# Optimization experiments

Hardware: AMD Instinct MI355X
Metric: run time of the kernel (lower is better)

Reference implementation:

```python
import jax, jax.numpy as jnp
import numpy as np

E = 8           # ensemble size
D_IN = 512      # input_dim (state+action)
H = 1024        # hidden size, arch=[1024, 1024]
D_OUT = 1       # output_dim (Q value)
LN_EPS = 1e-5


def setup_inputs() -> dict:
    key = jax.random.key(0)
    ks = jax.random.split(key, 8)
    s1 = 1.0 / np.sqrt(D_IN)
    s2 = 1.0 / np.sqrt(H)
    return {
        "x": jax.random.normal(ks[0], (16384, D_IN), dtype=jnp.float32),
        # stacked per-ensemble parameters: leading axis E
        "W1": jax.random.uniform(ks[1], (E, D_IN, H), jnp.float32, -s1, s1),
        "b1": jax.random.uniform(ks[2], (E, H), jnp.float32, -s1, s1),
        "g1": jnp.ones((E, H), jnp.float32),
        "be1": jnp.zeros((E, H), jnp.float32),
        "W2": jax.random.uniform(ks[3], (E, H, H), jnp.float32, -s2, s2),
        "b2": jax.random.uniform(ks[4], (E, H), jnp.float32, -s2, s2),
        "g2": jnp.ones((E, H), jnp.float32),
        "be2": jnp.zeros((E, H), jnp.float32),
        "W3": jax.random.uniform(ks[5], (E, H, D_OUT), jnp.float32, -s2, s2),
        "b3": jax.random.uniform(ks[6], (E, D_OUT), jnp.float32, -s2, s2),
    }


def _layer_norm(h, g, b):
    # h: [E, B, H]; g, b: [E, H] -> broadcast over batch
    mu = jnp.mean(h, axis=-1, keepdims=True)
    var = jnp.mean(jnp.square(h - mu), axis=-1, keepdims=True)
    return (h - mu) * jax.lax.rsqrt(var + LN_EPS) * g[:, None, :] + b[:, None, :]


def reference(x, W1, b1, g1, be1, W2, b2, g2, be2, W3, b3):
    # Layer 1: all ensemble members as one batched GEMM on shared input
    h = jnp.einsum('bd,edh->ebh', x, W1) + b1[:, None, :]       # [E, B, H]
    h = jax.nn.relu(_layer_norm(h, g1, be1))
    # Layer 2
    h = jnp.einsum('ebd,edh->ebh', h, W2) + b2[:, None, :]      # [E, B, H]
    h = jax.nn.relu(_layer_norm(h, g2, be2))
    # Head (identity head activation)
    qs = jnp.einsum('ebd,edo->ebo', h, W3) + b3[:, None, :]      # [E, B, 1]
    q = jnp.min(qs, axis=0)                                      # [B, 1]
    return (q, qs)
```

## Files before the change

### kernel.cpp

```cpp
#include <hip/hip_runtime.h>
#include <hip/hip_bf16.h>
#include <stdint.h>

#define EN    8
#define DIN   512
#define HID   1024
#define BATCH 16384
#define LN_EPS 1e-5f

typedef __bf16   bf16x8 __attribute__((ext_vector_type(8)));
typedef float    f32x4  __attribute__((ext_vector_type(4)));
typedef uint16_t u16x8  __attribute__((ext_vector_type(8)));
typedef uint16_t u16x4  __attribute__((ext_vector_type(4)));
typedef float    fl4    __attribute__((ext_vector_type(4)));

__device__ __forceinline__ uint16_t f2bf(float f) {
  uint32_t x = __builtin_bit_cast(uint32_t, f);
  uint32_t r = (x + 0x7fffu + ((x >> 16) & 1u)) >> 16;
  return (uint16_t)r;
}
__device__ __forceinline__ float bf2f(uint16_t u) {
  return __builtin_bit_cast(float, (uint32_t)u << 16);
}

__device__ __forceinline__ void gload16(const uint16_t* g, char* lds_d) {
  __builtin_amdgcn_global_load_lds(
      (const __attribute__((address_space(1))) uint32_t*)g,
      (__attribute__((address_space(3))) uint32_t*)lds_d, 16, 0, 0);
}

__device__ __forceinline__ f32x4 MF(bf16x8 a, bf16x8 b, f32x4 c) {
  return __builtin_amdgcn_mfma_f32_16x16x32_bf16(a, b, c, 0, 0, 0);
}

__global__ __launch_bounds__(256) void cvt_bf16(const float* __restrict__ src,
                                                uint16_t* __restrict__ dst, long n) {
  long i = ((long)blockIdx.x * 256 + threadIdx.x) * 4;
  if (i >= n) return;
  fl4 v = *(const fl4*)(src + i);
  u16x4 o;
  #pragma unroll
  for (int j = 0; j < 4; ++j) o[j] = f2bf(v[j]);
  *(u16x4*)(dst + i) = o;
}

__global__ __launch_bounds__(256) void transpose_cvt(const float* __restrict__ src,
                                                     uint16_t* __restrict__ dst,
                                                     int R, int C) {
  __shared__ float tile[32][33];
  const int e = blockIdx.z;
  const int c0 = blockIdx.x * 32;
  const int r0 = blockIdx.y * 32;
  const int tx = threadIdx.x & 31, ty = threadIdx.x >> 5;
  const float* s = src + (size_t)e * R * C;
  uint16_t*    d = dst + (size_t)e * R * C;
  #pragma unroll
  for (int i = 0; i < 32; i += 8)
    tile[ty + i][tx] = s[(size_t)(r0 + ty + i) * C + (c0 + tx)];
  __syncthreads();
  #pragma unroll
  for (int i = 0; i < 32; i += 8)
    d[(size_t)(c0 + ty + i) * R + (r0 + tx)] = f2bf(tile[tx][ty + i]);
}

__global__ __launch_bounds__(512, 2) void gemm256(
    const uint16_t* __restrict__ A, size_t a_estride,
    const uint16_t* __restrict__ Bt,
    const float*    __restrict__ bias,
    uint16_t*       __restrict__ C,
    int M, int K) {
  __shared__ __attribute__((aligned(16))) char lds[131072];
  const int tid = threadIdx.x;
  const int bx  = blockIdx.x;
  const int e   = bx & 7;
  const int t   = bx >> 3;
  const int mt  = t >> 2;
  const int nt  = t & 3;
  const int NT  = K >> 6;
  const int HT  = NT * 4;

  const uint16_t* Ae = A + (size_t)e * a_estride + (size_t)(mt * 256) * K;
  const uint16_t* Be = Bt + ((size_t)e * HID + nt * 256) * K;

  const int l  = tid & 63, wid = tid >> 6;
  const int wr = wid >> 2, wc = wid & 3;
  const int fr = l & 15, kq = l >> 4, f7 = fr & 7;

  const int srow = tid >> 3;
  const int su   = (tid & 7) ^ (srow & 7);
  const uint16_t* sA0 = Ae + (size_t)srow * K + su * 8;
  const uint16_t* sB0 = Be + (size_t)srow * K + su * 8;
  char* const dst0 = lds + tid * 16;

  const int rdA = wr * 8192 + fr * 128 + ((kq ^ f7) << 4);
  const int rdB = ((wc < 2) ? 16384 : 32768) + (wc & 1) * 8192 + fr * 128 + ((kq ^ f7) << 4);

  f32x4 acc[8][4];
  #pragma unroll
  for (int i = 0; i < 8; ++i)
    #pragma unroll
    for (int j = 0; j < 4; ++j) acc[i][j] = (f32x4)0.0f;

  auto STAGE = [&](int H) {
    const int tH = H >> 2, w = H & 3;
    char* dst = dst0 + ((tH & 1) << 16) + (w << 14);
    const size_t ko = (size_t)tH << 6;
    switch (w) {
      case 0: gload16(sA0 + ko, dst);
              gload16(sA0 + (size_t)128 * K + ko, dst + 8192); break;
      case 1: gload16(sB0 + ko, dst);
              gload16(sB0 + (size_t)64 * K + ko, dst + 8192); break;
      case 2: gload16(sB0 + (size_t)128 * K + ko, dst);
              gload16(sB0 + (size_t)192 * K + ko, dst + 8192); break;
      default: gload16(sA0 + (size_t)64 * K + ko, dst);
               gload16(sA0 + (size_t)192 * K + ko, dst + 8192); break;
    }
  };

  int H = 0;
  for (; H < 7; ++H) STAGE(H);
  asm volatile("s_waitcnt vmcnt(6)" ::: "memory");
  asm volatile("s_barrier" ::: "memory");

  bf16x8 af[4][2], bv[4][2];
  for (int kt = 0; kt < NT; ++kt) {
    const char* rb = lds + ((kt & 1) << 16);
    #pragma unroll
    for (int mi = 0; mi < 4; ++mi) {
      af[mi][0] = *(const bf16x8*)(rb + (rdA + mi * 2048));
      af[mi][1] = *(const bf16x8*)(rb + ((rdA + mi * 2048) ^ 64));
    }
    #pragma unroll
    for (int ni = 0; ni < 2; ++ni) {
      bv[ni][0] = *(const bf16x8*)(rb + (rdB + ni * 2048));
      bv[ni][1] = *(const bf16x8*)(rb + ((rdB + ni * 2048) ^ 64));
    }
    if (H < HT) STAGE(H++);
    asm volatile("s_barrier" ::: "memory");
    __builtin_amdgcn_s_setprio(1);
    #pragma unroll
    for (int mi = 0; mi < 4; ++mi)
      #pragma unroll
      for (int ni = 0; ni < 2; ++ni) {
        acc[mi][ni] = MF(af[mi][0], bv[ni][0], acc[mi][ni]);
        acc[mi][ni] = MF(af[mi][1], bv[ni][1], acc[mi][ni]);
      }
    __builtin_amdgcn_s_setprio(0);
    asm volatile("s_barrier" ::: "memory");
    #pragma unroll
    for (int ni = 2; ni < 4; ++ni) {
      bv[ni][0] = *(const bf16x8*)(rb + (rdB + ni * 2048));
      bv[ni][1] = *(const bf16x8*)(rb + ((rdB + ni * 2048) ^ 64));
    }
    if (H < HT) STAGE(H++);
    asm volatile("s_barrier" ::: "memory");
    __builtin_amdgcn_s_setprio(1);
    #pragma unroll
    for (int mi = 0; mi < 4; ++mi)
      #pragma unroll
      for (int ni = 2; ni < 4; ++ni) {
        acc[mi][ni] = MF(af[mi][0], bv[ni][0], acc[mi][ni]);
        acc[mi][ni] = MF(af[mi][1], bv[ni][1], acc[mi][ni]);
      }
    __builtin_amdgcn_s_setprio(0);
    asm volatile("s_barrier" ::: "memory");
    #pragma unroll
    for (int mi = 0; mi < 4; ++mi) {
      af[mi][0] = *(const bf16x8*)(rb + (rdA + 49152 + mi * 2048));
      af[mi][1] = *(const bf16x8*)(rb + ((rdA + 49152 + mi * 2048) ^ 64));
    }
    if (H < HT) STAGE(H++);
    asm volatile("s_barrier" ::: "memory");
    __builtin_amdgcn_s_setprio(1);
    #pragma unroll
    for (int mi = 0; mi < 4; ++mi)
      #pragma unroll
      for (int ni = 0; ni < 2; ++ni) {
        acc[mi + 4][ni] = MF(af[mi][0], bv[ni][0], acc[mi + 4][ni]);
        acc[mi + 4][ni] = MF(af[mi][1], bv[ni][1], acc[mi + 4][ni]);
      }
    __builtin_amdgcn_s_setprio(0);
    asm volatile("s_barrier" ::: "memory");
    if (H < HT) STAGE(H++);
    asm volatile("s_barrier" ::: "memory");
    __builtin_amdgcn_s_setprio(1);
    #pragma unroll
    for (int mi = 0; mi < 4; ++mi)
      #pragma unroll
      for (int ni = 2; ni < 4; ++ni) {
        acc[mi + 4][ni] = MF(af[mi][0], bv[ni][0], acc[mi + 4][ni]);
        acc[mi + 4][ni] = MF(af[mi][1], bv[ni][1], acc[mi + 4][ni]);
      }
    __builtin_amdgcn_s_setprio(0);
    if (kt < NT - 2)       asm volatile("s_waitcnt vmcnt(6)" ::: "memory");
    else if (kt == NT - 2) asm volatile("s_waitcnt vmcnt(0)" ::: "memory");
    asm volatile("s_barrier" ::: "memory");
  }

  const int col0 = nt * 256 + wc * 64 + fr;
  const int row0 = mt * 256 + wr * 128 + kq * 4;
  float bvv[4];
  #pragma unroll
  for (int ni = 0; ni < 4; ++ni) bvv[ni] = bias[(size_t)e * HID + col0 + ni * 16];
  #pragma unroll
  for (int mi = 0; mi < 8; ++mi) {
    #pragma unroll
    for (int i = 0; i < 4; ++i) {
      const int rg = row0 + mi * 16 + i;
      uint16_t* cp = C + ((size_t)e * M + rg) * HID + col0;
      #pragma unroll
      for (int ni = 0; ni < 4; ++ni)
        cp[ni * 16] = f2bf(acc[mi][ni][i] + bvv[ni]);
    }
  }
}

__global__ __launch_bounds__(256) void ln_relu(uint16_t* __restrict__ h,
                                               const float* __restrict__ g,
                                               const float* __restrict__ be,
                                               int kshift) {
  const int wid = threadIdx.x >> 6, l = threadIdx.x & 63;
  const long row = (long)blockIdx.x * 4 + wid;
  const int e = (int)(row >> kshift);
  uint16_t* p = h + row * HID;

  u16x8 s0 = *(const u16x8*)(p + l * 8);
  u16x8 s1 = *(const u16x8*)(p + 512 + l * 8);
  float v[16];
  #pragma unroll
  for (int j = 0; j < 8; ++j) { v[j] = bf2f(s0[j]); v[8 + j] = bf2f(s1[j]); }

  float sum = 0.f, sq = 0.f;
  #pragma unroll
  for (int j = 0; j < 16; ++j) { sum += v[j]; sq += v[j] * v[j]; }
  #pragma unroll
  for (int m = 1; m < 64; m <<= 1) {
    sum += __shfl_xor(sum, m);
    sq  += __shfl_xor(sq, m);
  }
  const float mu  = sum * (1.0f / HID);
  const float var = sq * (1.0f / HID) - mu * mu;
  const float rs  = rsqrtf(var + LN_EPS);

  const float* gp = g  + (size_t)e * HID;
  const float* bp = be + (size_t)e * HID;
  u16x8 o0, o1;
  #pragma unroll
  for (int j = 0; j < 8; ++j) {
    const int c0 = l * 8 + j, c1 = 512 + l * 8 + j;
    float x0 = (v[j]     - mu) * rs * gp[c0] + bp[c0];
    float x1 = (v[8 + j] - mu) * rs * gp[c1] + bp[c1];
    o0[j] = f2bf(fmaxf(x0, 0.f));
    o1[j] = f2bf(fmaxf(x1, 0.f));
  }
  *(u16x8*)(p + l * 8) = o0;
  *(u16x8*)(p + 512 + l * 8) = o1;
}

__global__ __launch_bounds__(256) void ln_head(const uint16_t* __restrict__ h,
                                               const float* __restrict__ g,
                                               const float* __restrict__ be,
                                               const float* __restrict__ W3,
                                               const float* __restrict__ b3,
                                               float* __restrict__ out,
                                               int b0, int CB) {
  __shared__ float qsh[EN];
  const int wv = threadIdx.x >> 6, l = threadIdx.x & 63;
  const long b = blockIdx.x;
  #pragma unroll
  for (int ee = 0; ee < 2; ++ee) {
    const int e = wv + ee * 4;
    const uint16_t* p = h + ((size_t)e * CB + b) * HID;
    u16x8 s0 = *(const u16x8*)(p + l * 8);
    u16x8 s1 = *(const u16x8*)(p + 512 + l * 8);
    float v[16];
    #pragma unroll
    for (int j = 0; j < 8; ++j) { v[j] = bf2f(s0[j]); v[8 + j] = bf2f(s1[j]); }
    float sum = 0.f, sq = 0.f;
    #pragma unroll
    for (int j = 0; j < 16; ++j) { sum += v[j]; sq += v[j] * v[j]; }
    #pragma unroll
    for (int m = 1; m < 64; m <<= 1) {
      sum += __shfl_xor(sum, m);
      sq  += __shfl_xor(sq, m);
    }
    const float mu  = sum * (1.0f / HID);
    const float var = sq * (1.0f / HID) - mu * mu;
    const float rs  = rsqrtf(var + LN_EPS);
    const float* gp = g  + (size_t)e * HID;
    const float* bp = be + (size_t)e * HID;
    const float* w  = W3 + (size_t)e * HID;
    float dot = 0.f;
    #pragma unroll
    for (int j = 0; j < 8; ++j) {
      const int c0 = l * 8 + j, c1 = 512 + l * 8 + j;
      float x0 = fmaxf((v[j]     - mu) * rs * gp[c0] + bp[c0], 0.f);
      float x1 = fmaxf((v[8 + j] - mu) * rs * gp[c1] + bp[c1], 0.f);
      dot += x0 * w[c0] + x1 * w[c1];
    }
    #pragma unroll
    for (int m = 1; m < 64; m <<= 1) dot += __shfl_xor(dot, m);
    if (l == 0) {
      const float qe = dot + b3[e];
      qsh[e] = qe;
      out[BATCH + (size_t)e * BATCH + b0 + b] = qe;
    }
  }
  __syncthreads();
  if (threadIdx.x == 0) {
    float m = qsh[0];
    #pragma unroll
    for (int i = 1; i < EN; ++i) m = fminf(m, qsh[i]);
    out[b0 + b] = m;
  }
}

extern "C" void kernel_launch(void* const* d_in, const int* in_sizes, int n_in,
                              void* d_out, int out_size, void* d_ws, size_t ws_size,
                              hipStream_t stream) {
  const float* x   = (const float*)d_in[0];
  const float* W1  = (const float*)d_in[1];
  const float* b1  = (const float*)d_in[2];
  const float* g1  = (const float*)d_in[3];
  const float* be1 = (const float*)d_in[4];
  const float* W2  = (const float*)d_in[5];
  const float* b2  = (const float*)d_in[6];
  const float* g2  = (const float*)d_in[7];
  const float* be2 = (const float*)d_in[8];
  const float* W3  = (const float*)d_in[9];
  const float* b3  = (const float*)d_in[10];
  float* out = (float*)d_out;

  char* ws = (char*)d_ws;
  uint16_t* xb  = (uint16_t*)ws; ws += (size_t)BATCH * DIN * 2;
  uint16_t* w1t = (uint16_t*)ws; ws += (size_t)EN * DIN * HID * 2;
  uint16_t* w2t = (uint16_t*)ws; ws += (size_t)EN * HID * HID * 2;
  size_t fixed = (size_t)(ws - (char*)d_ws);

  size_t avail = (ws_size > fixed) ? (ws_size - fixed) : 0;
  const size_t per_row = 2ULL * EN * HID * 2ULL;
  int CB = BATCH;
  while (CB > 256 && (size_t)CB * per_row > avail) CB >>= 1;
  const int nchunks = BATCH / CB;
  const int kshift = __builtin_ctz(CB);

  uint16_t* h1 = (uint16_t*)ws; ws += (size_t)EN * CB * HID * 2;
  uint16_t* h2 = (uint16_t*)ws;

  cvt_bf16<<<(BATCH * DIN / 4 + 255) / 256, 256, 0, stream>>>(x, xb, (long)BATCH * DIN);
  transpose_cvt<<<dim3(HID / 32, DIN / 32, EN), 256, 0, stream>>>(W1, w1t, DIN, HID);
  transpose_cvt<<<dim3(HID / 32, HID / 32, EN), 256, 0, stream>>>(W2, w2t, HID, HID);

  const int gblocks = (CB / 256) * (HID / 256) * EN;

  for (int c = 0; c < nchunks; ++c) {
    const int b0 = c * CB;
    gemm256<<<gblocks, 512, 0, stream>>>(xb + (size_t)b0 * DIN, (size_t)0,
                                         w1t, b1, h1, CB, DIN);
    ln_relu<<<(EN * CB) / 4, 256, 0, stream>>>(h1, g1, be1, kshift);
    gemm256<<<gblocks, 512, 0, stream>>>(h1, (size_t)CB * HID,
                                         w2t, b2, h2, CB, HID);
    ln_head<<<CB, 256, 0, stream>>>(h2, g2, be2, W3, b3, out, b0, CB);
  }
}
```

Measured before the change: 683.2 us.

## Split GEMM main loop into eight phases with LDS-fragment prefetch interleaved

```diff
diff --git a/kernel.cpp b/kernel.cpp
--- a/kernel.cpp
+++ b/kernel.cpp
@@ -32,6 +32,9 @@
 __device__ __forceinline__ f32x4 MF(bf16x8 a, bf16x8 b, f32x4 c) {
   return __builtin_amdgcn_mfma_f32_16x16x32_bf16(a, b, c, 0, 0, 0);
 }
+
+#define SB0() __builtin_amdgcn_sched_barrier(0)
+__device__ __forceinline__ void BARRIER() { __builtin_amdgcn_s_barrier(); }
 
 __global__ __launch_bounds__(256) void cvt_bf16(const float* __restrict__ src,
                                                 uint16_t* __restrict__ dst, long n) {
@@ -119,82 +122,130 @@
 
   int H = 0;
   for (; H < 7; ++H) STAGE(H);
-  asm volatile("s_waitcnt vmcnt(6)" ::: "memory");
-  asm volatile("s_barrier" ::: "memory");
-
-  bf16x8 af[4][2], bv[4][2];
+  asm volatile("s_waitcnt vmcnt(8)");
+  SB0();
+  BARRIER();
+  SB0();
+
+  bf16x8 a0[4], a0x[4], a1[4], b01[2], b23[2];
+  {
+    const char* rb = lds;
+    #pragma unroll
+    for (int mi = 0; mi < 4; ++mi) a0[mi] = *(const bf16x8*)(rb + (rdA + mi * 2048));
+    #pragma unroll
+    for (int ni = 0; ni < 2; ++ni) b01[ni] = *(const bf16x8*)(rb + (rdB + ni * 2048));
+  }
+
   for (int kt = 0; kt < NT; ++kt) {
-    const char* rb = lds + ((kt & 1) << 16);
-    #pragma unroll
-    for (int mi = 0; mi < 4; ++mi) {
-      af[mi][0] = *(const bf16x8*)(rb + (rdA + mi * 2048));
-      af[mi][1] = *(const bf16x8*)(rb + ((rdA + mi * 2048) ^ 64));
-    }
-    #pragma unroll
-    for (int ni = 0; ni < 2; ++ni) {
-      bv[ni][0] = *(const bf16x8*)(rb + (rdB + ni * 2048));
-      bv[ni][1] = *(const bf16x8*)(rb + ((rdB + ni * 2048) ^ 64));
-    }
+    const char* rb  = lds + ((kt & 1) << 16);
+    const char* rbn = lds + (((kt + 1) & 1) << 16);
+    const bool stg = true;
+    #define PHASE_SYNC(P_EVEN)                                        \
+      do {                                                            \
+        if (kt < NT - 2) { asm volatile("s_waitcnt vmcnt(8)"); }      \
+        SB0();                                                        \
+        BARRIER();                                                    \
+        SB0();                                                        \
+      } while (0)
+
+    #pragma unroll
+    for (int ni = 0; ni < 2; ++ni) b23[ni] = *(const bf16x8*)(rb + (rdB + (ni + 2) * 2048));
     if (H < HT) STAGE(H++);
-    asm volatile("s_barrier" ::: "memory");
-    __builtin_amdgcn_s_setprio(1);
-    #pragma unroll
-    for (int mi = 0; mi < 4; ++mi)
-      #pragma unroll
-      for (int ni = 0; ni < 2; ++ni) {
-        acc[mi][ni] = MF(af[mi][0], bv[ni][0], acc[mi][ni]);
-        acc[mi][ni] = MF(af[mi][1], bv[ni][1], acc[mi][ni]);
-      }
-    __builtin_amdgcn_s_setprio(0);
-    asm volatile("s_barrier" ::: "memory");
-    #pragma unroll
-    for (int ni = 2; ni < 4; ++ni) {
-      bv[ni][0] = *(const bf16x8*)(rb + (rdB + ni * 2048));
-      bv[ni][1] = *(const bf16x8*)(rb + ((rdB + ni * 2048) ^ 64));
-    }
+    __builtin_amdgcn_s_setprio(1);
+    #pragma unroll
+    for (int mi = 0; mi < 4; ++mi)
+      #pragma unroll
+      for (int ni = 0; ni < 2; ++ni) acc[mi][ni] = MF(a0[mi], b01[ni], acc[mi][ni]);
+    __builtin_amdgcn_s_setprio(0);
+    if (kt < NT - 2) { asm volatile("s_waitcnt vmcnt(8)"); }
+    else if (kt == NT - 2) { asm volatile("s_waitcnt vmcnt(0)"); }
+    SB0(); BARRIER(); SB0();
+
+    #pragma unroll
+    for (int mi = 0; mi < 4; ++mi) a1[mi] = *(const bf16x8*)(rb + (rdA + 49152 + mi * 2048));
+    #pragma unroll
+    for (int mi = 0; mi < 4; ++mi) a0x[mi] = *(const bf16x8*)(rb + ((rdA + mi * 2048) ^ 64));
+    __builtin_amdgcn_s_setprio(1);
+    #pragma unroll
+    for (int mi = 0; mi < 4; ++mi)
+      #pragma unroll
+      for (int ni = 2; ni < 4; ++ni) acc[mi][ni] = MF(a0[mi], b23[ni - 2], acc[mi][ni]);
+    __builtin_amdgcn_s_setprio(0);
+    if (kt < NT - 2) { asm volatile("s_waitcnt vmcnt(8)"); }
+    SB0(); BARRIER(); SB0();
+
     if (H < HT) STAGE(H++);
-    asm volatile("s_barrier" ::: "memory");
-    __builtin_amdgcn_s_setprio(1);
-    #pragma unroll
-    for (int mi = 0; mi < 4; ++mi)
-      #pragma unroll
-      for (int ni = 2; ni < 4; ++ni) {
-        acc[mi][ni] = MF(af[mi][0], bv[ni][0], acc[mi][ni]);
-        acc[mi][ni] = MF(af[mi][1], bv[ni][1], acc[mi][ni]);
-      }
-    __builtin_amdgcn_s_setprio(0);
-    asm volatile("s_barrier" ::: "memory");
-    #pragma unroll
-    for (int mi = 0; mi < 4; ++mi) {
-      af[mi][0] = *(const bf16x8*)(rb + (rdA + 49152 + mi * 2048));
-      af[mi][1] = *(const bf16x8*)(rb + ((rdA + 49152 + mi * 2048) ^ 64));
-    }
+    __builtin_amdgcn_s_setprio(1);
+    #pragma unroll
+    for (int mi = 0; mi < 4; ++mi)
+      #pragma unroll
+      for (int ni = 0; ni < 2; ++ni) acc[mi + 4][ni] = MF(a1[mi], b01[ni], acc[mi + 4][ni]);
+    __builtin_amdgcn_s_setprio(0);
+    if (kt < NT - 2) { asm volatile("s_waitcnt vmcnt(8)"); }
+    SB0(); BARRIER(); SB0();
+
+    #pragma unroll
+    for (int ni = 0; ni < 2; ++ni) b01[ni] = *(const bf16x8*)(rb + ((rdB + ni * 2048) ^ 64));
+    __builtin_amdgcn_s_setprio(1);
+    #pragma unroll
+    for (int mi = 0; mi < 4; ++mi)
+      #pragma unroll
+      for (int ni = 2; ni < 4; ++ni) acc[mi + 4][ni] = MF(a1[mi], b23[ni - 2], acc[mi + 4][ni]);
+    __builtin_amdgcn_s_setprio(0);
+    if (kt < NT - 2) { asm volatile("s_waitcnt vmcnt(8)"); }
+    SB0(); BARRIER(); SB0();
+
+    #pragma unroll
+    for (int ni = 0; ni < 2; ++ni) b23[ni] = *(const bf16x8*)(rb + ((rdB + (ni + 2) * 2048) ^ 64));
     if (H < HT) STAGE(H++);
-    asm volatile("s_barrier" ::: "memory");
-    __builtin_amdgcn_s_setprio(1);
-    #pragma unroll
-    for (int mi = 0; mi < 4; ++mi)
-      #pragma unroll
-      for (int ni = 0; ni < 2; ++ni) {
-        acc[mi + 4][ni] = MF(af[mi][0], bv[ni][0], acc[mi + 4][ni]);
-        acc[mi + 4][ni] = MF(af[mi][1], bv[ni][1], acc[mi + 4][ni]);
-      }
-    __builtin_amdgcn_s_setprio(0);
-    asm volatile("s_barrier" ::: "memory");
+    __builtin_amdgcn_s_setprio(1);
+    #pragma unroll
+    for (int mi = 0; mi < 4; ++mi)
+      #pragma unroll
+      for (int ni = 0; ni < 2; ++ni) acc[mi][ni] = MF(a0x[mi], b01[ni], acc[mi][ni]);
+    __builtin_amdgcn_s_setprio(0);
+    if (kt < NT - 2) { asm volatile("s_waitcnt vmcnt(8)"); }
+    SB0(); BARRIER(); SB0();
+
+    #pragma unroll
+    for (int mi = 0; mi < 4; ++mi) a1[mi] = *(const bf16x8*)(rb + ((rdA + 49152 + mi * 2048) ^ 64));
+    __builtin_amdgcn_s_setprio(1);
+    #pragma unroll
+    for (int mi = 0; mi < 4; ++mi)
+      #pragma unroll
+      for (int ni = 2; ni < 4; ++ni) acc[mi][ni] = MF(a0x[mi], b23[ni - 2], acc[mi][ni]);
+    __builtin_amdgcn_s_setprio(0);
+    if (kt < NT - 2) { asm volatile("s_waitcnt vmcnt(8)"); }
+    SB0(); BARRIER(); SB0();
+
+    if (kt + 1 < NT) {
+      #pragma unroll
+      for (int mi = 0; mi < 4; ++mi) a0[mi] = *(const bf16x8*)(rbn + (rdA + mi * 2048));
+    }
     if (H < HT) STAGE(H++);
-    asm volatile("s_barrier" ::: "memory");
-    __builtin_amdgcn_s_setprio(1);
-    #pragma unroll
-    for (int mi = 0; mi < 4; ++mi)
-      #pragma unroll
-      for (int ni = 2; ni < 4; ++ni) {
-        acc[mi + 4][ni] = MF(af[mi][0], bv[ni][0], acc[mi + 4][ni]);
-        acc[mi + 4][ni] = MF(af[mi][1], bv[ni][1], acc[mi + 4][ni]);
-      }
-    __builtin_amdgcn_s_setprio(0);
-    if (kt < NT - 2)       asm volatile("s_waitcnt vmcnt(6)" ::: "memory");
-    else if (kt == NT - 2) asm volatile("s_waitcnt vmcnt(0)" ::: "memory");
-    asm volatile("s_barrier" ::: "memory");
+    __builtin_amdgcn_s_setprio(1);
+    #pragma unroll
+    for (int mi = 0; mi < 4; ++mi)
+      #pragma unroll
+      for (int ni = 0; ni < 2; ++ni) acc[mi + 4][ni] = MF(a1[mi], b01[ni], acc[mi + 4][ni]);
+    __builtin_amdgcn_s_setprio(0);
+    if (kt < NT - 2) { asm volatile("s_waitcnt vmcnt(8)"); }
+    SB0(); BARRIER(); SB0();
+
+    if (kt + 1 < NT) {
+      #pragma unroll
+      for (int ni = 0; ni < 2; ++ni) b01[ni] = *(const bf16x8*)(rbn + (rdB + ni * 2048));
+    }
+    __builtin_amdgcn_s_setprio(1);
+    #pragma unroll
+    for (int mi = 0; mi < 4; ++mi)
+      #pragma unroll
+      for (int ni = 2; ni < 4; ++ni) acc[mi + 4][ni] = MF(a1[mi], b23[ni - 2], acc[mi + 4][ni]);
+    __builtin_amdgcn_s_setprio(0);
+    if (kt < NT - 2) { asm volatile("s_waitcnt vmcnt(8)"); }
+    SB0(); BARRIER(); SB0();
+    (void)stg;
+    #undef PHASE_SYNC
   }
 
   const int col0 = nt * 256 + wc * 64 + fr;
```

After: 683.0 us. About the same (-0.0%).
